# Performance work log

Hardware: AMD Instinct MI355X
Metric: run time of the kernel (lower is better)

The kernel has to match this reference:

```python
import jax, jax.numpy as jnp
import numpy as np

B, F, N, S, D = 128, 3, 64, 96, 64  # batch, features, nodes, steps, d_model
DIN = F + 1  # delta_t channel appended inside forward


def _layer_norm(x, g, b, eps=1e-5):
    mu = jnp.mean(x, -1, keepdims=True)
    var = jnp.mean((x - mu) ** 2, -1, keepdims=True)
    return (x - mu) * jax.lax.rsqrt(var + eps) * g + b


def _encoder_layer(x, inw, inb, ow, ob, w1, b1, w2, b2, g1, be1, g2, be2):
    # x: (B, N, D). Torch post-norm TransformerEncoderLayer, nhead=1, eval mode (no dropout).
    q, k, v = jnp.split(x @ inw.T + inb, 3, axis=-1)
    scores = jnp.einsum('bnd,bmd->bnm', q, k) / jnp.sqrt(jnp.asarray(D, x.dtype))
    a = jnp.einsum('bnm,bmd->bnd', jax.nn.softmax(scores, -1), v) @ ow.T + ob
    x = _layer_norm(x + a, g1, be1)
    ff = jax.nn.relu(x @ w1.T + b1) @ w2.T + b2
    return _layer_norm(x + ff, g2, be2)


def _diff_conv(x, adj, w, b):
    x1 = jnp.einsum('bcv,wv->bcw', x, adj)
    x2 = jnp.einsum('bcv,wv->bcw', x1, adj)
    z = jnp.concatenate([x, x1, x2], axis=1)  # (B, 3C, N)
    return jnp.einsum('bcn,oc->bon', z, w) + b[None, :, None]


def _forward(x, adj, h0, tp, uw, ub, cw, cb):
    times = x[:, 2, 0, :]  # (B, S) timestamps
    dt = jnp.concatenate([jnp.zeros((B, 1), x.dtype), times[:, 1:] - times[:, :-1]], axis=1)  # (B, S)
    xs = (jnp.transpose(x, (3, 0, 1, 2)), jnp.transpose(dt)[:, :, None])  # (S,B,F,N), (S,B,1)

    def step(h, inp):
        xt, d = inp  # (B,F,N), (B,1)
        xin = jnp.concatenate([xt, jnp.broadcast_to(d[:, :, None], (B, 1, N))], axis=1)  # (B,DIN,N)
        y = jnp.transpose(h, (0, 2, 1))  # (B, N, D): nodes are the attention sequence
        for i in range(2):
            y = _encoder_layer(y, *(a[i] for a in tp))
        eps = jnp.transpose(y, (0, 2, 1))  # (B, D, N)
        hd = jnp.sqrt(1.0 - d)[:, :, None] * h - jnp.sqrt(d)[:, :, None] * eps
        xg = jnp.concatenate([xin, hd], axis=1)  # (B, DIN+D, N)
        u = jax.nn.sigmoid(_diff_conv(xg, adj, uw, ub))
        c = jnp.tanh(_diff_conv(xg, adj, cw, cb))
        hn = u * hd + (1.0 - u) * c
        return hn, hn

    _, outs = jax.lax.scan(step, h0, xs)  # (S, B, D, N)
    return jnp.transpose(outs, (1, 3, 2, 0))  # (B, N, D, S) == stack().permute(1,3,2,0)


def setup_inputs() -> dict:
    key = jax.random.key(0)
    ks = jax.random.split(key, 12)
    s = 0.05
    x = jax.random.normal(ks[0], (B, F, N, S), jnp.float32)
    inc = jax.random.uniform(ks[1], (B, S), jnp.float32, 0.001, 0.01)
    x = x.at[:, 2, 0, :].set(jnp.cumsum(inc, axis=1))  # monotone times, delta_t in (0, 0.01)
    adj = jax.random.uniform(ks[2], (N, N), jnp.float32)
    adj = adj / jnp.sum(adj, axis=1, keepdims=True)
    h0 = jax.random.normal(ks[3], (B, D, N), jnp.float32)
    lengths = jax.random.randint(ks[4], (B,), 1, S, jnp.int32)  # unused by forward
    return {
        'x': x, 'adj': adj, 'lengths': lengths, 'h0': h0,
        't_inw': jax.random.normal(ks[5], (2, 3 * D, D), jnp.float32) * s,
        't_inb': jnp.zeros((2, 3 * D), jnp.float32),
        't_ow': jax.random.normal(ks[6], (2, D, D), jnp.float32) * s,
        't_ob': jnp.zeros((2, D), jnp.float32),
        't_w1': jax.random.normal(ks[7], (2, 64, D), jnp.float32) * s,
        't_b1': jnp.zeros((2, 64), jnp.float32),
        't_w2': jax.random.normal(ks[8], (2, D, 64), jnp.float32) * s,
        't_b2': jnp.zeros((2, D), jnp.float32),
        't_g1': jnp.ones((2, D), jnp.float32), 't_be1': jnp.zeros((2, D), jnp.float32),
        't_g2': jnp.ones((2, D), jnp.float32), 't_be2': jnp.zeros((2, D), jnp.float32),
        'uw': jax.random.normal(ks[9], (D, 3 * (DIN + D)), jnp.float32) * s,
        'ub': jnp.zeros((D,), jnp.float32),
        'cw': jax.random.normal(ks[10], (D, 3 * (DIN + D)), jnp.float32) * s,
        'cb': jnp.zeros((D,), jnp.float32),
    }


def reference(x, adj, lengths, h0, t_inw, t_inb, t_ow, t_ob, t_w1, t_b1, t_w2, t_b2,
              t_g1, t_be1, t_g2, t_be2, uw, ub, cw, cb):
    tp = (t_inw, t_inb, t_ow, t_ob, t_w1, t_b1, t_w2, t_b2, t_g1, t_be1, t_g2, t_be2)
    return _forward(x, adj, h0, tp, uw, ub, cw, cb)
```

## Files before the change

### kernel.cpp

```cpp
#include <hip/hip_runtime.h>
#include <math.h>

#define TPB 512

typedef __attribute__((ext_vector_type(8))) short bf16x8;
typedef __attribute__((ext_vector_type(4))) float f32x4;
typedef unsigned short u16;

#define MFMA(a, b, c) __builtin_amdgcn_mfma_f32_16x16x32_bf16(a, b, c, 0, 0, 0)

__device__ __forceinline__ u16 f2bf(float f) {
  union { float f; unsigned u; } v; v.f = f;
  unsigned u = v.u;
  return (u16)((u + 0x7fffu + ((u >> 16) & 1u)) >> 16);
}
__device__ __forceinline__ float bf2f(u16 h) {
  union { unsigned u; float f; } v; v.u = ((unsigned)h) << 16; return v.f;
}
__device__ __forceinline__ unsigned cvt2(float a0, float a1) {
  return (unsigned)f2bf(a0) | ((unsigned)f2bf(a1) << 16);
}
__device__ __forceinline__ void cvt4u(float a0, float a1, float a2, float a3, u16 o[4]) {
  o[0] = f2bf(a0); o[1] = f2bf(a1); o[2] = f2bf(a2); o[3] = f2bf(a3);
}

__device__ __forceinline__ bf16x8 fragL(const u16* B, int row0, int pitch, int kb, int lane) {
  return *(const bf16x8*)(B + (row0 + (lane & 15)) * pitch + kb + ((lane >> 4) << 3));
}
__device__ __forceinline__ bf16x8 fragG(const float* __restrict__ W, int row0, int stride,
                                        int kb, int lane) {
  const float* p = W + (size_t)(row0 + (lane & 15)) * stride + kb + ((lane >> 4) << 3);
  float4 a = *(const float4*)p, b = *(const float4*)(p + 4);
  bf16x8 r;
  r[0] = (short)f2bf(a.x); r[1] = (short)f2bf(a.y); r[2] = (short)f2bf(a.z); r[3] = (short)f2bf(a.w);
  r[4] = (short)f2bf(b.x); r[5] = (short)f2bf(b.y); r[6] = (short)f2bf(b.z); r[7] = (short)f2bf(b.w);
  return r;
}
template<int PREW>
__device__ __forceinline__ bf16x8 wfrag(const float* __restrict__ Wg,
                                        const u16* __restrict__ Wp,
                                        int m, int f, int kh, int lane) {
  if constexpr (PREW)
    return *(const bf16x8*)(Wp + (size_t)m * 4096 + f * 1024 + kh * 512 + lane * 8);
  else
    return fragG(Wg, f * 16, 64, kh * 32, lane);
}

__global__ __launch_bounds__(256)
void prep_kernel(const float* __restrict__ t_inw, const float* __restrict__ t_ow,
                 const float* __restrict__ t_w1, const float* __restrict__ t_w2,
                 const float* __restrict__ adj, const float* __restrict__ x,
                 u16* __restrict__ wp, u16* __restrict__ wpA2,
                 float* __restrict__ wsDT, u16* __restrict__ wsX) {
  int m = blockIdx.x;
  if (m == 12) {
    __shared__ float a2[4096];
    for (int e = threadIdx.x; e < 4096; e += 256) {
      int w = e >> 6, u = e & 63;
      float sum = 0.f;
      for (int v = 0; v < 64; ++v) sum += adj[w * 64 + v] * adj[v * 64 + u];
      a2[e] = sum;
    }
    __syncthreads();
    for (int t = threadIdx.x; t < 4096; t += 256) {
      int j = t & 7, ln = (t >> 3) & 63, kh = (t >> 9) & 1, f = t >> 10;
      int row = f * 16 + (ln & 15);
      int k = kh * 32 + ((ln >> 4) << 3) + j;
      wpA2[t] = f2bf(a2[row * 64 + k]);
    }
    return;
  }
  if (m >= 13) {
    int b = m - 13;
    const float* times = x + ((size_t)b * 3 + 2) * 64 * 96;
    for (int i = threadIdx.x; i < 96 * 256; i += 256) {
      int s = i >> 8, idx = i & 255, f = idx >> 6, n = idx & 63;
      float v;
      if (f < 3) v = x[(((size_t)b * 3 + f) * 64 + n) * 96 + s];
      else {
        float dt = s ? (times[s] - times[s - 1]) : 0.f;
        v = dt;
        if (n == 0) wsDT[b * 96 + s] = dt;
      }
      wsX[((size_t)b * 96 + s) * 256 + idx] = f2bf(v);
    }
    return;
  }
  int l = m / 6, r = m % 6;
  const float* W;
  if (r < 3)       W = t_inw + l * 12288 + r * 4096;
  else if (r == 3) W = t_ow + l * 4096;
  else if (r == 4) W = t_w1 + l * 4096;
  else             W = t_w2 + l * 4096;
  for (int t = threadIdx.x; t < 4096; t += 256) {
    int j = t & 7, ln = (t >> 3) & 63, kh = (t >> 9) & 1, f = t >> 10;
    int row = f * 16 + (ln & 15);
    int k = kh * 32 + ((ln >> 4) << 3) + j;
    wp[(size_t)m * 4096 + t] = f2bf(W[row * 64 + k]);
  }
}

__global__ __launch_bounds__(TPB, 2)
void gcrnn_fast(const float* __restrict__ adj,
                const float* __restrict__ h0,
                const float* __restrict__ t_inb, const float* __restrict__ t_ob,
                const float* __restrict__ t_b1,  const float* __restrict__ t_b2,
                const float* __restrict__ t_g1,  const float* __restrict__ t_be1,
                const float* __restrict__ t_g2,  const float* __restrict__ t_be2,
                const float* __restrict__ uw,    const float* __restrict__ ub,
                const float* __restrict__ cw,    const float* __restrict__ cb,
                const u16* __restrict__ wsW,  const u16* __restrict__ wsA2,
                const float* __restrict__ wsDT, const u16* __restrict__ wsX,
                float* __restrict__ wsOut)
{
  const int b = blockIdx.x;
  const int tid = threadIdx.x;
  const int wv = tid >> 6;
  const int lane = tid & 63;
  const int lx = lane & 15;
  const int gq = (lane >> 4) << 2;
  const int rs = wv & 3;
  const int of0 = (wv >> 2) * 2;
  const int fA = wv >> 2;

  __shared__ __align__(16) u16 adjB[64 * 72];
  __shared__ __align__(16) u16 Y0[64 * 72];
  __shared__ __align__(16) u16 Y1[64 * 72];
  __shared__ __align__(16) u16 Qb[64 * 72];
  __shared__ __align__(16) u16 Kb[64 * 72];
  __shared__ __align__(16) u16 VTb[64 * 72];
  __shared__ __align__(16) u16 Pb[64 * 72];
  __shared__ __align__(16) u16 xgB[80 * 72];
  __shared__ __align__(16) u16 zTB[64 * 232];
  __shared__ __align__(16) u16 uwcwB[2 * 4 * 7 * 512];

  float hreg[2][4];
  {
    const int nb = rs * 16 + gq;
#pragma unroll
    for (int ff = 0; ff < 2; ++ff) {
      int o = (of0 + ff) * 16 + lx;
      float4 hv = *(const float4*)(h0 + (size_t)b * 4096 + o * 64 + nb);
#pragma unroll
      for (int j = 0; j < 4; ++j) {
        hreg[ff][j] = (&hv.x)[j];
        Y0[(nb + j) * 72 + o] = f2bf(hreg[ff][j]);
      }
    }
  }
  for (int i = tid; i < 4096; i += TPB)
    adjB[(i >> 6) * 72 + (i & 63)] = f2bf(adj[i]);
  for (int i = tid; i < 2 * 4 * 7 * 512; i += TPB) {
    int t = i;
    int j = t & 7; t >>= 3;
    int ln = t & 63; t >>= 6;
    int kh = t % 7; t /= 7;
    int f = t & 3; int mat = t >> 2;
    int o = f * 16 + (ln & 15);
    int k = kh * 32 + ((ln >> 4) << 3) + j;
    const float* W = mat ? cw : uw;
    uwcwB[i] = (k < 204) ? f2bf(W[o * 204 + k]) : (u16)0;
  }
  for (int i = tid; i < 64 * 28; i += TPB)
    zTB[(i / 28) * 232 + 204 + (i % 28)] = 0;
  for (int i = tid; i < 12 * 72; i += TPB)
    xgB[68 * 72 + i] = 0;
  __syncthreads();

  const float buo = ub[of0 * 16 + lx], buo2 = ub[(of0 + 1) * 16 + lx];
  const float bco = cb[of0 * 16 + lx], bco2 = cb[(of0 + 1) * 16 + lx];
  float hdreg[2][4];

  for (int s = 0; s < 96; ++s) {
    float dcur = wsDT[b * 96 + s];
    float sq1 = sqrtf(1.f - dcur), sq2 = sqrtf(dcur);

    for (int l = 0; l < 2; ++l) {
      const int l6 = l * 6;
      const float* inb = t_inb + l * 192;
      const float* ob  = t_ob  + l * 64;
      const float* bb1 = t_b1  + l * 64;
      const float* bb2 = t_b2  + l * 64;
      const float* g1  = t_g1  + l * 64;
      const float* be1 = t_be1 + l * 64;
      const float* g2  = t_g2  + l * 64;
      const float* be2 = t_be2 + l * 64;

      bf16x8 fq[2][2], fk[2][2], fvr[2];
#pragma unroll
      for (int fi = 0; fi < 2; ++fi)
#pragma unroll
        for (int kh = 0; kh < 2; ++kh) {
          fq[fi][kh] = wfrag<1>(nullptr, wsW, l6 + 0, fA + fi * 2, kh, lane);
          fk[fi][kh] = wfrag<1>(nullptr, wsW, l6 + 1, fA + fi * 2, kh, lane);
        }
      if (wv >= 4) {
#pragma unroll
        for (int kh = 0; kh < 2; ++kh)
          fvr[kh] = wfrag<1>(nullptr, wsW, l6 + 2, rs, kh, lane);
      }

      {
        bf16x8 a0 = fragL(Y0, rs * 16, 72, 0, lane);
        bf16x8 a1 = fragL(Y0, rs * 16, 72, 32, lane);
#pragma unroll
        for (int fi = 0; fi < 2; ++fi) {
          int f = fA + fi * 2;
          int col = f * 16 + lx;
          {
            f32x4 acc = {0.f, 0.f, 0.f, 0.f};
            acc = MFMA(a0, fq[fi][0], acc);
            acc = MFMA(a1, fq[fi][1], acc);
            float bv = inb[col];
            u16 o4[4]; cvt4u(acc[0] + bv, acc[1] + bv, acc[2] + bv, acc[3] + bv, o4);
#pragma unroll
            for (int j = 0; j < 4; ++j)
              Qb[(rs * 16 + gq + j) * 72 + col] = o4[j];
          }
          {
            f32x4 acc = {0.f, 0.f, 0.f, 0.f};
            acc = MFMA(a0, fk[fi][0], acc);
            acc = MFMA(a1, fk[fi][1], acc);
            float bv = inb[64 + col];
            u16 o4[4]; cvt4u(acc[0] + bv, acc[1] + bv, acc[2] + bv, acc[3] + bv, o4);
#pragma unroll
            for (int j = 0; j < 4; ++j)
              Kb[(rs * 16 + gq + j) * 72 + col] = o4[j];
          }
        }
      }
      __syncthreads();

      if (wv < 4) {
        bf16x8 qa0 = fragL(Qb, rs * 16, 72, 0, lane);
        bf16x8 qa1 = fragL(Qb, rs * 16, 72, 32, lane);
        f32x4 sc[4];
#pragma unroll
        for (int f = 0; f < 4; ++f) {
          f32x4 acc = {0.f, 0.f, 0.f, 0.f};
          acc = MFMA(qa0, fragL(Kb, f * 16, 72, 0, lane), acc);
          acc = MFMA(qa1, fragL(Kb, f * 16, 72, 32, lane), acc);
#pragma unroll
          for (int j = 0; j < 4; ++j) acc[j] *= 0.125f;
          sc[f] = acc;
        }
#pragma unroll
        for (int j = 0; j < 4; ++j) {
          float m1 = fmaxf(fmaxf(sc[0][j], sc[1][j]), fmaxf(sc[2][j], sc[3][j]));
          m1 = fmaxf(m1, __shfl_xor(m1, 1));
          m1 = fmaxf(m1, __shfl_xor(m1, 2));
          m1 = fmaxf(m1, __shfl_xor(m1, 4));
          m1 = fmaxf(m1, __shfl_xor(m1, 8));
          float s1 = 0.f;
#pragma unroll
          for (int f = 0; f < 4; ++f) { float e = __expf(sc[f][j] - m1); sc[f][j] = e; s1 += e; }
          s1 += __shfl_xor(s1, 1); s1 += __shfl_xor(s1, 2);
          s1 += __shfl_xor(s1, 4); s1 += __shfl_xor(s1, 8);
          float inv = 1.f / s1;
          int row = rs * 16 + gq + j;
          u16 o4[4];
          cvt4u(sc[0][j] * inv, sc[1][j] * inv, sc[2][j] * inv, sc[3][j] * inv, o4);
#pragma unroll
          for (int f = 0; f < 4; ++f)
            Pb[row * 72 + f * 16 + lx] = o4[f];
        }
      } else {
#pragma unroll
        for (int f = 0; f < 4; ++f) {
          f32x4 acc = {0.f, 0.f, 0.f, 0.f};
          acc = MFMA(fvr[0], fragL(Y0, f * 16, 72, 0, lane), acc);
          acc = MFMA(fvr[1], fragL(Y0, f * 16, 72, 32, lane), acc);
          int dd0 = rs * 16 + gq;
          u16 o4[4];
          cvt4u(acc[0] + inb[128 + dd0], acc[1] + inb[128 + dd0 + 1],
                acc[2] + inb[128 + dd0 + 2], acc[3] + inb[128 + dd0 + 3], o4);
#pragma unroll
          for (int j = 0; j < 4; ++j)
            VTb[(dd0 + j) * 72 + f * 16 + lx] = o4[j];
        }
      }
      __syncthreads();

      if (wv < 4) {
        bf16x8 fo[4][2], fw1[4][2];
#pragma unroll
        for (int f = 0; f < 4; ++f)
#pragma unroll
          for (int kh = 0; kh < 2; ++kh) {
            fo[f][kh]  = wfrag<1>(nullptr, wsW, l6 + 3, f, kh, lane);
            fw1[f][kh] = wfrag<1>(nullptr, wsW, l6 + 4, f, kh, lane);
          }
        {
          bf16x8 pa0 = fragL(Pb, rs * 16, 72, 0, lane);
          bf16x8 pa1 = fragL(Pb, rs * 16, 72, 32, lane);
#pragma unroll
          for (int f = 0; f < 4; ++f) {
            f32x4 acc = {0.f, 0.f, 0.f, 0.f};
            acc = MFMA(pa0, fragL(VTb, f * 16, 72, 0, lane), acc);
            acc = MFMA(pa1, fragL(VTb, f * 16, 72, 32, lane), acc);
            u16 o4[4]; cvt4u(acc[0], acc[1], acc[2], acc[3], o4);
#pragma unroll
            for (int j = 0; j < 4; ++j)
              Qb[(rs * 16 + gq + j) * 72 + f * 16 + lx] = o4[j];
          }
        }
        {
          bf16x8 a0 = fragL(Qb, rs * 16, 72, 0, lane);
          bf16x8 a1 = fragL(Qb, rs * 16, 72, 32, lane);
          float t4[4][4];
#pragma unroll
          for (int f = 0; f < 4; ++f) {
            f32x4 acc = {0.f, 0.f, 0.f, 0.f};
            acc = MFMA(a0, fo[f][0], acc);
            acc = MFMA(a1, fo[f][1], acc);
            int col = f * 16 + lx;
            float bv = ob[col];
#pragma unroll
            for (int j = 0; j < 4; ++j) {
              int row = rs * 16 + gq + j;
              t4[f][j] = acc[j] + bv + bf2f(Y0[row * 72 + col]);
            }
          }
#pragma unroll
          for (int j = 0; j < 4; ++j) {
            float s1 = t4[0][j] + t4[1][j] + t4[2][j] + t4[3][j];
            float s2 = t4[0][j] * t4[0][j] + t4[1][j] * t4[1][j]
                     + t4[2][j] * t4[2][j] + t4[3][j] * t4[3][j];
            s1 += __shfl_xor(s1, 1); s2 += __shfl_xor(s2, 1);
            s1 += __shfl_xor(s1, 2); s2 += __shfl_xor(s2, 2);
            s1 += __shfl_xor(s1, 4); s2 += __shfl_xor(s2, 4);
            s1 += __shfl_xor(s1, 8); s2 += __shfl_xor(s2, 8);
            float mu = s1 * 0.015625f;
            float rstd = rsqrtf(s2 * 0.015625f - mu * mu + 1e-5f);
            int row = rs * 16 + gq + j;
            u16 o4[4];
            cvt4u((t4[0][j] - mu) * rstd * g1[0 * 16 + lx] + be1[0 * 16 + lx],
                  (t4[1][j] - mu) * rstd * g1[1 * 16 + lx] + be1[1 * 16 + lx],
                  (t4[2][j] - mu) * rstd * g1[2 * 16 + lx] + be1[2 * 16 + lx],
                  (t4[3][j] - mu) * rstd * g1[3 * 16 + lx] + be1[3 * 16 + lx], o4);
#pragma unroll
            for (int f = 0; f < 4; ++f)
              Y1[row * 72 + f * 16 + lx] = o4[f];
          }
        }
        {
          bf16x8 a0 = fragL(Y1, rs * 16, 72, 0, lane);
          bf16x8 a1 = fragL(Y1, rs * 16, 72, 32, lane);
#pragma unroll
          for (int f = 0; f < 4; ++f) {
            f32x4 acc = {0.f, 0.f, 0.f, 0.f};
            acc = MFMA(a0, fw1[f][0], acc);
            acc = MFMA(a1, fw1[f][1], acc);
            int col = f * 16 + lx;
            float bv = bb1[col];
            u16 o4[4];
            cvt4u(fmaxf(acc[0] + bv, 0.f), fmaxf(acc[1] + bv, 0.f),
                  fmaxf(acc[2] + bv, 0.f), fmaxf(acc[3] + bv, 0.f), o4);
#pragma unroll
            for (int j = 0; j < 4; ++j)
              Kb[(rs * 16 + gq + j) * 72 + col] = o4[j];
          }
        }
        if (l == 0) {
          bf16x8 fw2[4][2];
#pragma unroll
          for (int f = 0; f < 4; ++f)
#pragma unroll
            for (int kh = 0; kh < 2; ++kh)
              fw2[f][kh] = wfrag<1>(nullptr, wsW, l6 + 5, f, kh, lane);
          bf16x8 a0 = fragL(Kb, rs * 16, 72, 0, lane);
          bf16x8 a1 = fragL(Kb, rs * 16, 72, 32, lane);
          float t4[4][4];
#pragma unroll
          for (int f = 0; f < 4; ++f) {
            f32x4 acc = {0.f, 0.f, 0.f, 0.f};
            acc = MFMA(a0, fw2[f][0], acc);
            acc = MFMA(a1, fw2[f][1], acc);
            int col = f * 16 + lx;
            float bv = bb2[col];
#pragma unroll
            for (int j = 0; j < 4; ++j) {
              int row = rs * 16 + gq + j;
              t4[f][j] = acc[j] + bv + bf2f(Y1[row * 72 + col]);
            }
          }
#pragma unroll
          for (int j = 0; j < 4; ++j) {
            float s1 = t4[0][j] + t4[1][j] + t4[2][j] + t4[3][j];
            float s2 = t4[0][j] * t4[0][j] + t4[1][j] * t4[1][j]
                     + t4[2][j] * t4[2][j] + t4[3][j] * t4[3][j];
            s1 += __shfl_xor(s1, 1); s2 += __shfl_xor(s2, 1);
            s1 += __shfl_xor(s1, 2); s2 += __shfl_xor(s2, 2);
            s1 += __shfl_xor(s1, 4); s2 += __shfl_xor(s2, 4);
            s1 += __shfl_xor(s1, 8); s2 += __shfl_xor(s2, 8);
            float mu = s1 * 0.015625f;
            float rstd = rsqrtf(s2 * 0.015625f - mu * mu + 1e-5f);
            int row = rs * 16 + gq + j;
            u16 o4[4];
            cvt4u((t4[0][j] - mu) * rstd * g2[0 * 16 + lx] + be2[0 * 16 + lx],
                  (t4[1][j] - mu) * rstd * g2[1 * 16 + lx] + be2[1 * 16 + lx],
                  (t4[2][j] - mu) * rstd * g2[2 * 16 + lx] + be2[2 * 16 + lx],
                  (t4[3][j] - mu) * rstd * g2[3 * 16 + lx] + be2[3 * 16 + lx], o4);
#pragma unroll
            for (int f = 0; f < 4; ++f)
              Y0[row * 72 + f * 16 + lx] = o4[f];
          }
        }
      }
      __syncthreads();

      if (l == 1) {
        bf16x8 fw2[4][2];
#pragma unroll
        for (int f = 0; f < 4; ++f)
#pragma unroll
          for (int kh = 0; kh < 2; ++kh)
            fw2[f][kh] = wfrag<1>(nullptr, wsW, l6 + 5, f, kh, lane);
        bf16x8 a0 = fragL(Kb, rs * 16, 72, 0, lane);
        bf16x8 a1 = fragL(Kb, rs * 16, 72, 32, lane);
        float t4[4][4];
#pragma unroll
        for (int f = 0; f < 4; ++f) {
          f32x4 acc = {0.f, 0.f, 0.f, 0.f};
          acc = MFMA(a0, fw2[f][0], acc);
          acc = MFMA(a1, fw2[f][1], acc);
          int col = f * 16 + lx;
          float bv = bb2[col];
#pragma unroll
          for (int j = 0; j < 4; ++j) {
            int row = rs * 16 + gq + j;
            t4[f][j] = acc[j] + bv + bf2f(Y1[row * 72 + col]);
          }
        }
#pragma unroll
        for (int j = 0; j < 4; ++j) {
          float s1 = t4[0][j] + t4[1][j] + t4[2][j] + t4[3][j];
          float s2 = t4[0][j] * t4[0][j] + t4[1][j] * t4[1][j]
                   + t4[2][j] * t4[2][j] + t4[3][j] * t4[3][j];
          s1 += __shfl_xor(s1, 1); s2 += __shfl_xor(s2, 1);
          s1 += __shfl_xor(s1, 2); s2 += __shfl_xor(s2, 2);
          s1 += __shfl_xor(s1, 4); s2 += __shfl_xor(s2, 4);
          s1 += __shfl_xor(s1, 8); s2 += __shfl_xor(s2, 8);
          float mu = s1 * 0.015625f;
          float rstd = rsqrtf(s2 * 0.015625f - mu * mu + 1e-5f);
#pragma unroll
          for (int f = 0; f < 4; ++f) {
            int col = f * 16 + lx;
            t4[f][j] = (t4[f][j] - mu) * rstd * g2[col] + be2[col];
          }
        }
        {
          const u16* xr = wsX + ((size_t)b * 96 + s) * 256;
          for (int i = tid; i < 256; i += TPB) {
            u16 v = xr[i];
            int f = i >> 6, n = i & 63;
            xgB[f * 72 + n] = v;
            zTB[n * 232 + f] = v;
          }
        }
        const int nb = rs * 16 + gq;
#pragma unroll
        for (int f = 0; f < 4; ++f) {
          if ((f >> 1) == (wv >> 2)) {
            const int ff = f & 1;
            int o = f * 16 + lx;
            float hd0 = sq1 * hreg[ff][0] - sq2 * t4[f][0];
            float hd1 = sq1 * hreg[ff][1] - sq2 * t4[f][1];
            float hd2 = sq1 * hreg[ff][2] - sq2 * t4[f][2];
            float hd3 = sq1 * hreg[ff][3] - sq2 * t4[f][3];
            hdreg[ff][0] = hd0; hdreg[ff][1] = hd1;
            hdreg[ff][2] = hd2; hdreg[ff][3] = hd3;
            unsigned p0 = cvt2(hd0, hd1), p1 = cvt2(hd2, hd3);
            zTB[(nb + 0) * 232 + 4 + o] = (u16)p0;
            zTB[(nb + 1) * 232 + 4 + o] = (u16)(p0 >> 16);
            zTB[(nb + 2) * 232 + 4 + o] = (u16)p1;
            zTB[(nb + 3) * 232 + 4 + o] = (u16)(p1 >> 16);
            uint2 pk; pk.x = p0; pk.y = p1;
            *(uint2*)(xgB + (4 + o) * 72 + nb) = pk;
          }
        }
        __syncthreads();
      }
    }

    {
      f32x4 aU0 = {0.f,0.f,0.f,0.f}, aU1 = {0.f,0.f,0.f,0.f};
      f32x4 aC0 = {0.f,0.f,0.f,0.f}, aC1 = {0.f,0.f,0.f,0.f};
      bf16x8 g0 = *(const bf16x8*)(wsA2 + rs * 1024 + lane * 8);
      bf16x8 g1 = *(const bf16x8*)(wsA2 + rs * 1024 + 512 + lane * 8);
      bf16x8 aj0 = fragL(adjB, rs * 16, 72, 0, lane);
      bf16x8 aj1 = fragL(adjB, rs * 16, 72, 32, lane);

#define HT(A0, A1, CF, OFF) { \
      f32x4 acc = {0.f,0.f,0.f,0.f}; \
      acc = MFMA(A0, fragL(xgB, (CF) * 16, 72, 0, lane), acc); \
      acc = MFMA(A1, fragL(xgB, (CF) * 16, 72, 32, lane), acc); \
      int c = (CF) * 16 + lx; \
      if (c < 68) { u16 o4[4]; cvt4u(acc[0], acc[1], acc[2], acc[3], o4); \
        _Pragma("unroll") for (int j = 0; j < 4; ++j) \
          zTB[(rs * 16 + gq + j) * 232 + (OFF) + c] = o4[j]; } }

      HT(aj0, aj1, 0, 68); HT(aj0, aj1, 1, 68); HT(aj0, aj1, 2, 68);
      HT(aj0, aj1, 3, 68); HT(aj0, aj1, 4, 68);
#pragma unroll
      for (int kh = 0; kh < 2; ++kh) {
        bf16x8 a = fragL(zTB, rs * 16, 232, kh * 32, lane);
        {
          const u16* pu = uwcwB + (size_t)((of0 + 0) * 7 + kh) * 512 + lane * 8;
          const u16* pc = uwcwB + (size_t)((4 + of0 + 0) * 7 + kh) * 512 + lane * 8;
          aU0 = MFMA(a, *(const bf16x8*)pu, aU0);
          aC0 = MFMA(a, *(const bf16x8*)pc, aC0);
        }
        {
          const u16* pu = uwcwB + (size_t)((of0 + 1) * 7 + kh) * 512 + lane * 8;
          const u16* pc = uwcwB + (size_t)((4 + of0 + 1) * 7 + kh) * 512 + lane * 8;
          aU1 = MFMA(a, *(const bf16x8*)pu, aU1);
          aC1 = MFMA(a, *(const bf16x8*)pc, aC1);
        }
      }
      HT(g0, g1, 0, 136); HT(g0, g1, 1, 136); HT(g0, g1, 2, 136);
      HT(g0, g1, 3, 136); HT(g0, g1, 4, 136);
#undef HT

#pragma unroll
      for (int kh = 2; kh < 7; ++kh) {
        bf16x8 a = fragL(zTB, rs * 16, 232, kh * 32, lane);
        {
          const u16* pu = uwcwB + (size_t)((of0 + 0) * 7 + kh) * 512 + lane * 8;
          const u16* pc = uwcwB + (size_t)((4 + of0 + 0) * 7 + kh) * 512 + lane * 8;
          aU0 = MFMA(a, *(const bf16x8*)pu, aU0);
          aC0 = MFMA(a, *(const bf16x8*)pc, aC0);
        }
        {
          const u16* pu = uwcwB + (size_t)((of0 + 1) * 7 + kh) * 512 + lane * 8;
          const u16* pc = uwcwB + (size_t)((4 + of0 + 1) * 7 + kh) * 512 + lane * 8;
          aU1 = MFMA(a, *(const bf16x8*)pu, aU1);
          aC1 = MFMA(a, *(const bf16x8*)pc, aC1);
        }
      }
      const int nb = rs * 16 + gq;
#pragma unroll
      for (int ff = 0; ff < 2; ++ff) {
        f32x4 aU = ff ? aU1 : aU0;
        f32x4 aC = ff ? aC1 : aC0;
        float bu_ = ff ? buo2 : buo;
        float bc_ = ff ? bco2 : bco;
        int o = (of0 + ff) * 16 + lx;
        float4 ov;
#pragma unroll
        for (int j = 0; j < 4; ++j) {
          float u = 1.f / (1.f + __expf(-(aU[j] + bu_)));
          float z = aC[j] + bc_;
          z = fminf(fmaxf(z, -15.f), 15.f);
          float e2 = __expf(2.f * z);
          float cval = (e2 - 1.f) / (e2 + 1.f);
          float hn = u * hdreg[ff][j] + (1.f - u) * cval;
          hreg[ff][j] = hn;
          (&ov.x)[j] = hn;
        }
        unsigned pk0 = cvt2(ov.x, ov.y), pk1 = cvt2(ov.z, ov.w);
        Y0[(nb + 0) * 72 + o] = (u16)pk0;
        Y0[(nb + 1) * 72 + o] = (u16)(pk0 >> 16);
        Y0[(nb + 2) * 72 + o] = (u16)pk1;
        Y0[(nb + 3) * 72 + o] = (u16)(pk1 >> 16);
        *(float4*)(wsOut + ((size_t)b * 96 + s) * 4096 + o * 64 + nb) = ov;
      }
    }
    __syncthreads();
  }
}

__global__ __launch_bounds__(TPB, 2)
void gcrnn_fb(const float* __restrict__ x, const float* __restrict__ adj,
              const float* __restrict__ h0,
              const float* __restrict__ t_inw, const float* __restrict__ t_inb,
              const float* __restrict__ t_ow,  const float* __restrict__ t_ob,
              const float* __restrict__ t_w1,  const float* __restrict__ t_b1,
              const float* __restrict__ t_w2,  const float* __restrict__ t_b2,
              const float* __restrict__ t_g1,  const float* __restrict__ t_be1,
              const float* __restrict__ t_g2,  const float* __restrict__ t_be2,
              const float* __restrict__ uw,    const float* __restrict__ ub,
              const float* __restrict__ cw,    const float* __restrict__ cb,
              float* __restrict__ out)
{
  const int b = blockIdx.x;
  const int tid = threadIdx.x;
  const int wv = tid >> 6;
  const int lane = tid & 63;
  const int lx = lane & 15;
  const int gq = (lane >> 4) << 2;
  const int rs = wv & 3;
  const int of0 = (wv >> 2) * 2;
  const int fA = wv >> 2;

  __shared__ __align__(16) u16 adjB[64 * 72];
  __shared__ __align__(16) u16 adj2B[64 * 72];
  __shared__ __align__(16) u16 ysB[64 * 72];
  __shared__ __align__(16) u16 pool[4 * 4608];
  __shared__ __align__(16) u16 zTB[64 * 232];
  __shared__ __align__(16) u16 uwcwB[2 * 4 * 7 * 512];

  u16* Qb  = pool;
  u16* Kb  = pool + 4608;
  u16* VTb = pool + 9216;
  u16* Pb  = pool + 13824;
  u16* xgB = pool;

  float hreg[2][4];
  {
    const int nb = rs * 16 + gq;
#pragma unroll
    for (int ff = 0; ff < 2; ++ff) {
      int o = (of0 + ff) * 16 + lx;
      float4 hv = *(const float4*)(h0 + (size_t)b * 4096 + o * 64 + nb);
#pragma unroll
      for (int j = 0; j < 4; ++j) {
        hreg[ff][j] = (&hv.x)[j];
        ysB[(nb + j) * 72 + o] = f2bf(hreg[ff][j]);
      }
    }
  }
  for (int i = tid; i < 4096; i += TPB)
    adjB[(i >> 6) * 72 + (i & 63)] = f2bf(adj[i]);
  for (int i = tid; i < 4096; i += TPB) {
    int w = i >> 6, u = i & 63;
    float sum = 0.f;
    for (int v = 0; v < 64; ++v) sum += adj[w * 64 + v] * adj[v * 64 + u];
    adj2B[w * 72 + u] = f2bf(sum);
  }
  for (int i = tid; i < 2 * 4 * 7 * 512; i += TPB) {
    int t = i;
    int j = t & 7; t >>= 3;
    int ln = t & 63; t >>= 6;
    int kh = t % 7; t /= 7;
    int f = t & 3; int mat = t >> 2;
    int o = f * 16 + (ln & 15);
    int k = kh * 32 + ((ln >> 4) << 3) + j;
    const float* W = mat ? cw : uw;
    uwcwB[i] = (k < 204) ? f2bf(W[o * 204 + k]) : (u16)0;
  }
  for (int i = tid; i < 64 * 28; i += TPB)
    zTB[(i / 28) * 232 + 204 + (i % 28)] = 0;
  __syncthreads();

  const float* times = x + ((size_t)b * 3 + 2) * 64 * 96;
  float hdreg[2][4];

  for (int s = 0; s < 96; ++s) {
    float dcur = (s == 0) ? 0.f : (times[s] - times[s - 1]);
    float sq1 = sqrtf(1.f - dcur), sq2 = sqrtf(dcur);

    for (int l = 0; l < 2; ++l) {
      const float* inw = t_inw + l * 12288;
      const float* inb = t_inb + l * 192;
      const float* ow  = t_ow  + l * 4096;
      const float* ob  = t_ob  + l * 64;
      const float* w1  = t_w1  + l * 4096;
      const float* bb1 = t_b1  + l * 64;
      const float* w2  = t_w2  + l * 4096;
      const float* bb2 = t_b2  + l * 64;
      const float* g1  = t_g1  + l * 64;
      const float* be1 = t_be1 + l * 64;
      const float* g2  = t_g2  + l * 64;
      const float* be2 = t_be2 + l * 64;

      {
        bf16x8 a0 = fragL(ysB, rs * 16, 72, 0, lane);
        bf16x8 a1 = fragL(ysB, rs * 16, 72, 32, lane);
#pragma unroll
        for (int fi = 0; fi < 2; ++fi) {
          int f = fA + fi * 2;
          int col = f * 16 + lx;
          {
            f32x4 acc = {0.f, 0.f, 0.f, 0.f};
            acc = MFMA(a0, fragG(inw, f * 16, 64, 0, lane), acc);
            acc = MFMA(a1, fragG(inw, f * 16, 64, 32, lane), acc);
            float bv = inb[col];
            u16 o4[4]; cvt4u(acc[0] + bv, acc[1] + bv, acc[2] + bv, acc[3] + bv, o4);
#pragma unroll
            for (int j = 0; j < 4; ++j)
              Qb[(rs * 16 + gq + j) * 72 + col] = o4[j];
          }
          {
            f32x4 acc = {0.f, 0.f, 0.f, 0.f};
            acc = MFMA(a0, fragG(inw + 4096, f * 16, 64, 0, lane), acc);
            acc = MFMA(a1, fragG(inw + 4096, f * 16, 64, 32, lane), acc);
            float bv = inb[64 + col];
            u16 o4[4]; cvt4u(acc[0] + bv, acc[1] + bv, acc[2] + bv, acc[3] + bv, o4);
#pragma unroll
            for (int j = 0; j < 4; ++j)
              Kb[(rs * 16 + gq + j) * 72 + col] = o4[j];
          }
        }
      }
      __syncthreads();

      if (wv < 4) {
        bf16x8 qa0 = fragL(Qb, rs * 16, 72, 0, lane);
        bf16x8 qa1 = fragL(Qb, rs * 16, 72, 32, lane);
        f32x4 sc[4];
#pragma unroll
        for (int f = 0; f < 4; ++f) {
          f32x4 acc = {0.f, 0.f, 0.f, 0.f};
          acc = MFMA(qa0, fragL(Kb, f * 16, 72, 0, lane), acc);
          acc = MFMA(qa1, fragL(Kb, f * 16, 72, 32, lane), acc);
#pragma unroll
          for (int j = 0; j < 4; ++j) acc[j] *= 0.125f;
          sc[f] = acc;
        }
#pragma unroll
        for (int j = 0; j < 4; ++j) {
          float m1 = fmaxf(fmaxf(sc[0][j], sc[1][j]), fmaxf(sc[2][j], sc[3][j]));
          m1 = fmaxf(m1, __shfl_xor(m1, 1));
          m1 = fmaxf(m1, __shfl_xor(m1, 2));
          m1 = fmaxf(m1, __shfl_xor(m1, 4));
          m1 = fmaxf(m1, __shfl_xor(m1, 8));
          float s1 = 0.f;
#pragma unroll
          for (int f = 0; f < 4; ++f) { float e = __expf(sc[f][j] - m1); sc[f][j] = e; s1 += e; }
          s1 += __shfl_xor(s1, 1); s1 += __shfl_xor(s1, 2);
          s1 += __shfl_xor(s1, 4); s1 += __shfl_xor(s1, 8);
          float inv = 1.f / s1;
          int row = rs * 16 + gq + j;
          u16 o4[4];
          cvt4u(sc[0][j] * inv, sc[1][j] * inv, sc[2][j] * inv, sc[3][j] * inv, o4);
#pragma unroll
          for (int f = 0; f < 4; ++f)
            Pb[row * 72 + f * 16 + lx] = o4[f];
        }
      } else {
        bf16x8 wa0 = fragG(inw + 8192, rs * 16, 64, 0, lane);
        bf16x8 wa1 = fragG(inw + 8192, rs * 16, 64, 32, lane);
#pragma unroll
        for (int f = 0; f < 4; ++f) {
          f32x4 acc = {0.f, 0.f, 0.f, 0.f};
          acc = MFMA(wa0, fragL(ysB, f * 16, 72, 0, lane), acc);
          acc = MFMA(wa1, fragL(ysB, f * 16, 72, 32, lane), acc);
          int dd0 = rs * 16 + gq;
          u16 o4[4];
          cvt4u(acc[0] + inb[128 + dd0], acc[1] + inb[128 + dd0 + 1],
                acc[2] + inb[128 + dd0 + 2], acc[3] + inb[128 + dd0 + 3], o4);
#pragma unroll
          for (int j = 0; j < 4; ++j)
            VTb[(dd0 + j) * 72 + f * 16 + lx] = o4[j];
        }
      }
      __syncthreads();

      {
        bf16x8 pa0 = fragL(Pb, rs * 16, 72, 0, lane);
        bf16x8 pa1 = fragL(Pb, rs * 16, 72, 32, lane);
#pragma unroll
        for (int fi = 0; fi < 2; ++fi) {
          int f = fA + fi * 2;
          f32x4 acc = {0.f, 0.f, 0.f, 0.f};
          acc = MFMA(pa0, fragL(VTb, f * 16, 72, 0, lane), acc);
          acc = MFMA(pa1, fragL(VTb, f * 16, 72, 32, lane), acc);
          u16 o4[4]; cvt4u(acc[0], acc[1], acc[2], acc[3], o4);
#pragma unroll
          for (int j = 0; j < 4; ++j)
            Qb[(rs * 16 + gq + j) * 72 + f * 16 + lx] = o4[j];
        }
      }
      __syncthreads();

      if (wv < 4) {
        bf16x8 a0 = fragL(Qb, rs * 16, 72, 0, lane);
        bf16x8 a1 = fragL(Qb, rs * 16, 72, 32, lane);
        float t4[4][4];
#pragma unroll
        for (int f = 0; f < 4; ++f) {
          f32x4 acc = {0.f, 0.f, 0.f, 0.f};
          acc = MFMA(a0, fragG(ow, f * 16, 64, 0, lane), acc);
          acc = MFMA(a1, fragG(ow, f * 16, 64, 32, lane), acc);
          int col = f * 16 + lx;
          float bv = ob[col];
#pragma unroll
          for (int j = 0; j < 4; ++j) {
            int row = rs * 16 + gq + j;
            t4[f][j] = acc[j] + bv + bf2f(ysB[row * 72 + col]);
          }
        }
#pragma unroll
        for (int j = 0; j < 4; ++j) {
          float s1 = t4[0][j] + t4[1][j] + t4[2][j] + t4[3][j];
          float s2 = t4[0][j] * t4[0][j] + t4[1][j] * t4[1][j]
                   + t4[2][j] * t4[2][j] + t4[3][j] * t4[3][j];
          s1 += __shfl_xor(s1, 1); s2 += __shfl_xor(s2, 1);
          s1 += __shfl_xor(s1, 2); s2 += __shfl_xor(s2, 2);
          s1 += __shfl_xor(s1, 4); s2 += __shfl_xor(s2, 4);
          s1 += __shfl_xor(s1, 8); s2 += __shfl_xor(s2, 8);
          float mu = s1 * 0.015625f;
          float rstd = rsqrtf(s2 * 0.015625f - mu * mu + 1e-5f);
          int row = rs * 16 + gq + j;
          u16 o4[4];
          cvt4u((t4[0][j] - mu) * rstd * g1[0 * 16 + lx] + be1[0 * 16 + lx],
                (t4[1][j] - mu) * rstd * g1[1 * 16 + lx] + be1[1 * 16 + lx],
                (t4[2][j] - mu) * rstd * g1[2 * 16 + lx] + be1[2 * 16 + lx],
                (t4[3][j] - mu) * rstd * g1[3 * 16 + lx] + be1[3 * 16 + lx], o4);
#pragma unroll
          for (int f = 0; f < 4; ++f)
            ysB[row * 72 + f * 16 + lx] = o4[f];
        }
      }
      __syncthreads();

      {
        bf16x8 a0 = fragL(ysB, rs * 16, 72, 0, lane);
        bf16x8 a1 = fragL(ysB, rs * 16, 72, 32, lane);
#pragma unroll
        for (int fi = 0; fi < 2; ++fi) {
          int f = fA + fi * 2;
          f32x4 acc = {0.f, 0.f, 0.f, 0.f};
          acc = MFMA(a0, fragG(w1, f * 16, 64, 0, lane), acc);
          acc = MFMA(a1, fragG(w1, f * 16, 64, 32, lane), acc);
          int col = f * 16 + lx;
          float bv = bb1[col];
          u16 o4[4];
          cvt4u(fmaxf(acc[0] + bv, 0.f), fmaxf(acc[1] + bv, 0.f),
                fmaxf(acc[2] + bv, 0.f), fmaxf(acc[3] + bv, 0.f), o4);
#pragma unroll
          for (int j = 0; j < 4; ++j)
            Kb[(rs * 16 + gq + j) * 72 + col] = o4[j];
        }
      }
      __syncthreads();

      if (wv < 4) {
        bf16x8 a0 = fragL(Kb, rs * 16, 72, 0, lane);
        bf16x8 a1 = fragL(Kb, rs * 16, 72, 32, lane);
        float t4[4][4];
#pragma unroll
        for (int f = 0; f < 4; ++f) {
          f32x4 acc = {0.f, 0.f, 0.f, 0.f};
          acc = MFMA(a0, fragG(w2, f * 16, 64, 0, lane), acc);
          acc = MFMA(a1, fragG(w2, f * 16, 64, 32, lane), acc);
          int col = f * 16 + lx;
          float bv = bb2[col];
#pragma unroll
          for (int j = 0; j < 4; ++j) {
            int row = rs * 16 + gq + j;
            t4[f][j] = acc[j] + bv + bf2f(ysB[row * 72 + col]);
          }
        }
#pragma unroll
        for (int j = 0; j < 4; ++j) {
          float s1 = t4[0][j] + t4[1][j] + t4[2][j] + t4[3][j];
          float s2 = t4[0][j] * t4[0][j] + t4[1][j] * t4[1][j]
                   + t4[2][j] * t4[2][j] + t4[3][j] * t4[3][j];
          s1 += __shfl_xor(s1, 1); s2 += __shfl_xor(s2, 1);
          s1 += __shfl_xor(s1, 2); s2 += __shfl_xor(s2, 2);
          s1 += __shfl_xor(s1, 4); s2 += __shfl_xor(s2, 4);
          s1 += __shfl_xor(s1, 8); s2 += __shfl_xor(s2, 8);
          float mu = s1 * 0.015625f;
          float rstd = rsqrtf(s2 * 0.015625f - mu * mu + 1e-5f);
          int row = rs * 16 + gq + j;
          u16 o4[4];
          cvt4u((t4[0][j] - mu) * rstd * g2[0 * 16 + lx] + be2[0 * 16 + lx],
                (t4[1][j] - mu) * rstd * g2[1 * 16 + lx] + be2[1 * 16 + lx],
                (t4[2][j] - mu) * rstd * g2[2 * 16 + lx] + be2[2 * 16 + lx],
                (t4[3][j] - mu) * rstd * g2[3 * 16 + lx] + be2[3 * 16 + lx], o4);
#pragma unroll
          for (int f = 0; f < 4; ++f)
            ysB[row * 72 + f * 16 + lx] = o4[f];
        }
      }
      __syncthreads();
    }

    {
      for (int i = tid; i < 256; i += TPB) {
        int f = i >> 6, n = i & 63;
        float v = (f < 3) ? x[(((size_t)b * 3 + f) * 64 + n) * 96 + s] : dcur;
        u16 v16 = f2bf(v);
        xgB[f * 72 + n] = v16;
        zTB[n * 232 + f] = v16;
      }
      const int nb = rs * 16 + gq;
#pragma unroll
      for (int ff = 0; ff < 2; ++ff) {
        int o = (of0 + ff) * 16 + lx;
        float hd0 = sq1 * hreg[ff][0] - sq2 * bf2f(ysB[(nb + 0) * 72 + o]);
        float hd1 = sq1 * hreg[ff][1] - sq2 * bf2f(ysB[(nb + 1) * 72 + o]);
        float hd2 = sq1 * hreg[ff][2] - sq2 * bf2f(ysB[(nb + 2) * 72 + o]);
        float hd3 = sq1 * hreg[ff][3] - sq2 * bf2f(ysB[(nb + 3) * 72 + o]);
        hdreg[ff][0] = hd0; hdreg[ff][1] = hd1; hdreg[ff][2] = hd2; hdreg[ff][3] = hd3;
        unsigned p0 = cvt2(hd0, hd1), p1 = cvt2(hd2, hd3);
        zTB[(nb + 0) * 232 + 4 + o] = (u16)p0;
        zTB[(nb + 1) * 232 + 4 + o] = (u16)(p0 >> 16);
        zTB[(nb + 2) * 232 + 4 + o] = (u16)p1;
        zTB[(nb + 3) * 232 + 4 + o] = (u16)(p1 >> 16);
        uint2 pk; pk.x = p0; pk.y = p1;
        *(uint2*)(xgB + (4 + o) * 72 + nb) = pk;
      }
    }
    __syncthreads();

    for (int t = wv; t < 40; t += 8) {
      int which = (t >= 20) ? 1 : 0;
      int tt = t - which * 20;
      int rw = tt & 3, cf = tt >> 2;
      const u16* A = which ? adj2B : adjB;
      f32x4 acc = {0.f, 0.f, 0.f, 0.f};
      acc = MFMA(fragL(A, rw * 16, 72, 0, lane), fragL(xgB, cf * 16, 72, 0, lane), acc);
      acc = MFMA(fragL(A, rw * 16, 72, 32, lane), fragL(xgB, cf * 16, 72, 32, lane), acc);
      int c = cf * 16 + lx;
      if (c < 68) {
        u16 o4[4]; cvt4u(acc[0], acc[1], acc[2], acc[3], o4);
#pragma unroll
        for (int j = 0; j < 4; ++j)
          zTB[(rw * 16 + gq + j) * 232 + 68 + which * 68 + c] = o4[j];
      }
    }
    __syncthreads();

    {
      f32x4 aU[2] = {{0.f,0.f,0.f,0.f},{0.f,0.f,0.f,0.f}};
      f32x4 aC[2] = {{0.f,0.f,0.f,0.f},{0.f,0.f,0.f,0.f}};
#pragma unroll
      for (int kh = 0; kh < 7; ++kh) {
        bf16x8 a = fragL(zTB, rs * 16, 232, kh * 32, lane);
#pragma unroll
        for (int ff = 0; ff < 2; ++ff) {
          int f = of0 + ff;
          const u16* pu = uwcwB + (size_t)((0 * 4 + f) * 7 + kh) * 512 + lane * 8;
          const u16* pc = uwcwB + (size_t)((1 * 4 + f) * 7 + kh) * 512 + lane * 8;
          aU[ff] = MFMA(a, *(const bf16x8*)pu, aU[ff]);
          aC[ff] = MFMA(a, *(const bf16x8*)pc, aC[ff]);
        }
      }
      const int nb = rs * 16 + gq;
#pragma unroll
      for (int ff = 0; ff < 2; ++ff) {
        int o = (of0 + ff) * 16 + lx;
        float bu_ = ub[o], bc_ = cb[o];
        float4 ov;
#pragma unroll
        for (int j = 0; j < 4; ++j) {
          float u = 1.f / (1.f + __expf(-(aU[ff][j] + bu_)));
          float z = aC[ff][j] + bc_;
          z = fminf(fmaxf(z, -15.f), 15.f);
          float e2 = __expf(2.f * z);
          float cval = (e2 - 1.f) / (e2 + 1.f);
          float hn = u * hdreg[ff][j] + (1.f - u) * cval;
          hreg[ff][j] = hn;
          (&ov.x)[j] = hn;
        }
        unsigned pk0 = cvt2(ov.x, ov.y), pk1 = cvt2(ov.z, ov.w);
        ysB[(nb + 0) * 72 + o] = (u16)pk0;
        ysB[(nb + 1) * 72 + o] = (u16)(pk0 >> 16);
        ysB[(nb + 2) * 72 + o] = (u16)pk1;
        ysB[(nb + 3) * 72 + o] = (u16)(pk1 >> 16);
#pragma unroll
        for (int j = 0; j < 4; ++j)
          out[((size_t)(b * 64 + (nb + j)) * 64 + o) * 96 + s] = (&ov.x)[j];
      }
    }
    __syncthreads();
  }
}

__global__ __launch_bounds__(256)
void transp_kernel(const float* __restrict__ ws, float* __restrict__ out) {
  int blk = blockIdx.x;
  int b = blk >> 6, o = blk & 63;
  __shared__ float t[96 * 68];
  for (int i = threadIdx.x; i < 96 * 64; i += 256) {
    int ss = i >> 6, n = i & 63;
    t[ss * 68 + n] = ws[((size_t)b * 96 + ss) * 4096 + o * 64 + n];
  }
  __syncthreads();
  for (int i = threadIdx.x; i < 64 * 96; i += 256) {
    int n = i / 96, ss = i - n * 96;
    out[((size_t)(b * 64 + n) * 64 + o) * 96 + ss] = t[ss * 68 + n];
  }
}

extern "C" void kernel_launch(void* const* d_in, const int* in_sizes, int n_in,
                              void* d_out, int out_size, void* d_ws, size_t ws_size,
                              hipStream_t stream)
{
  (void)in_sizes; (void)n_in; (void)out_size;
  const float* x     = (const float*)d_in[0];
  const float* adj   = (const float*)d_in[1];
  const float* h0    = (const float*)d_in[3];
  const float* t_inw = (const float*)d_in[4];
  const float* t_inb = (const float*)d_in[5];
  const float* t_ow  = (const float*)d_in[6];
  const float* t_ob  = (const float*)d_in[7];
  const float* t_w1  = (const float*)d_in[8];
  const float* t_b1  = (const float*)d_in[9];
  const float* t_w2  = (const float*)d_in[10];
  const float* t_b2  = (const float*)d_in[11];
  const float* t_g1  = (const float*)d_in[12];
  const float* t_be1 = (const float*)d_in[13];
  const float* t_g2  = (const float*)d_in[14];
  const float* t_be2 = (const float*)d_in[15];
  const float* uw    = (const float*)d_in[16];
  const float* ub    = (const float*)d_in[17];
  const float* cw    = (const float*)d_in[18];
  const float* cb    = (const float*)d_in[19];
  float* out = (float*)d_out;

  const size_t offA2    = 98304;
  const size_t offDT    = 106496;
  const size_t offX     = 155648;
  const size_t offStage = 6447104;
  const size_t stageBytes = (size_t)128 * 96 * 4096 * 4;

  if (ws_size >= offStage + stageBytes) {
    u16*   wsW   = (u16*)d_ws;
    u16*   wsA2  = (u16*)((char*)d_ws + offA2);
    float* wsDT  = (float*)((char*)d_ws + offDT);
    u16*   wsX   = (u16*)((char*)d_ws + offX);
    float* wsOut = (float*)((char*)d_ws + offStage);

    hipLaunchKernelGGL(prep_kernel, dim3(141), dim3(256), 0, stream,
                       t_inw, t_ow, t_w1, t_w2, adj, x, wsW, wsA2, wsDT, wsX);
    hipLaunchKernelGGL(gcrnn_fast, dim3(128), dim3(TPB), 0, stream,
                       adj, h0, t_inb, t_ob, t_b1, t_b2, t_g1, t_be1, t_g2, t_be2,
                       uw, ub, cw, cb, wsW, wsA2, wsDT, wsX, wsOut);
    hipLaunchKernelGGL(transp_kernel, dim3(128 * 64), dim3(256), 0, stream, wsOut, out);
  } else {
    hipLaunchKernelGGL(gcrnn_fb, dim3(128), dim3(TPB), 0, stream,
                       x, adj, h0, t_inw, t_inb, t_ow, t_ob, t_w1, t_b1,
                       t_w2, t_b2, t_g1, t_be1, t_g2, t_be2, uw, ub, cw, cb, out);
  }
}
```

Before: 1.447 ms.

## Rebalance QKV projection across waves and drop a per-layer barrier

Waves 0-3 now compute all of Q plus half of K, while waves 4-7 compute the other half of K and V^T in the same phase. V^T is therefore ready at the first barrier, so the separate barrier after the score/softmax phase is removed. The attention-output and FFN weight fragment loads are hoisted earlier to overlap latency. The FFN hidden buffer moves from Kb to Pb to avoid a hazard now that Kb is still being read. The bf16 conversion is also swapped for the HIP library intrinsic. Extra registers for the hoisted fragments may raise register pressure.

```diff
diff --git a/kernel.cpp b/kernel.cpp
--- a/kernel.cpp
+++ b/kernel.cpp
@@ -1,4 +1,5 @@
 #include <hip/hip_runtime.h>
+#include <hip/hip_bf16.h>
 #include <math.h>
 
 #define TPB 512
@@ -10,9 +11,8 @@
 #define MFMA(a, b, c) __builtin_amdgcn_mfma_f32_16x16x32_bf16(a, b, c, 0, 0, 0)
 
 __device__ __forceinline__ u16 f2bf(float f) {
-  union { float f; unsigned u; } v; v.f = f;
-  unsigned u = v.u;
-  return (u16)((u + 0x7fffu + ((u >> 16) & 1u)) >> 16);
+  __hip_bfloat16 h = __float2bfloat16(f);
+  return *reinterpret_cast<u16*>(&h);
 }
 __device__ __forceinline__ float bf2f(u16 h) {
   union { unsigned u; float f; } v; v.u = ((unsigned)h) << 16; return v.f;
@@ -121,7 +121,6 @@
   const int gq = (lane >> 4) << 2;
   const int rs = wv & 3;
   const int of0 = (wv >> 2) * 2;
-  const int fA = wv >> 2;
 
   __shared__ __align__(16) u16 adjB[64 * 72];
   __shared__ __align__(16) u16 Y0[64 * 72];
@@ -186,64 +185,107 @@
       const float* g2  = t_g2  + l * 64;
       const float* be2 = t_be2 + l * 64;
 
-      bf16x8 fq[2][2], fk[2][2], fvr[2];
-#pragma unroll
-      for (int fi = 0; fi < 2; ++fi)
-#pragma unroll
-        for (int kh = 0; kh < 2; ++kh) {
-          fq[fi][kh] = wfrag<1>(nullptr, wsW, l6 + 0, fA + fi * 2, kh, lane);
-          fk[fi][kh] = wfrag<1>(nullptr, wsW, l6 + 1, fA + fi * 2, kh, lane);
-        }
-      if (wv >= 4) {
-#pragma unroll
-        for (int kh = 0; kh < 2; ++kh)
-          fvr[kh] = wfrag<1>(nullptr, wsW, l6 + 2, rs, kh, lane);
-      }
-
       {
         bf16x8 a0 = fragL(Y0, rs * 16, 72, 0, lane);
         bf16x8 a1 = fragL(Y0, rs * 16, 72, 32, lane);
-#pragma unroll
-        for (int fi = 0; fi < 2; ++fi) {
-          int f = fA + fi * 2;
-          int col = f * 16 + lx;
-          {
+        if (wv < 4) {
+          bf16x8 fq[4][2], fkp[2][2];
+#pragma unroll
+          for (int f = 0; f < 4; ++f)
+#pragma unroll
+            for (int kh = 0; kh < 2; ++kh)
+              fq[f][kh] = wfrag<1>(nullptr, wsW, l6 + 0, f, kh, lane);
+#pragma unroll
+          for (int fi = 0; fi < 2; ++fi)
+#pragma unroll
+            for (int kh = 0; kh < 2; ++kh)
+              fkp[fi][kh] = wfrag<1>(nullptr, wsW, l6 + 1, fi * 2, kh, lane);
+#pragma unroll
+          for (int f = 0; f < 4; ++f) {
             f32x4 acc = {0.f, 0.f, 0.f, 0.f};
-            acc = MFMA(a0, fq[fi][0], acc);
-            acc = MFMA(a1, fq[fi][1], acc);
+            acc = MFMA(a0, fq[f][0], acc);
+            acc = MFMA(a1, fq[f][1], acc);
+            int col = f * 16 + lx;
             float bv = inb[col];
             u16 o4[4]; cvt4u(acc[0] + bv, acc[1] + bv, acc[2] + bv, acc[3] + bv, o4);
 #pragma unroll
             for (int j = 0; j < 4; ++j)
               Qb[(rs * 16 + gq + j) * 72 + col] = o4[j];
           }
-          {
+#pragma unroll
+          for (int fi = 0; fi < 2; ++fi) {
+            int f = fi * 2;
             f32x4 acc = {0.f, 0.f, 0.f, 0.f};
-            acc = MFMA(a0, fk[fi][0], acc);
-            acc = MFMA(a1, fk[fi][1], acc);
+            acc = MFMA(a0, fkp[fi][0], acc);
+            acc = MFMA(a1, fkp[fi][1], acc);
+            int col = f * 16 + lx;
             float bv = inb[64 + col];
             u16 o4[4]; cvt4u(acc[0] + bv, acc[1] + bv, acc[2] + bv, acc[3] + bv, o4);
 #pragma unroll
             for (int j = 0; j < 4; ++j)
               Kb[(rs * 16 + gq + j) * 72 + col] = o4[j];
           }
+        } else {
+          bf16x8 fkp[2][2], fvr[2];
+#pragma unroll
+          for (int fi = 0; fi < 2; ++fi)
+#pragma unroll
+            for (int kh = 0; kh < 2; ++kh)
+              fkp[fi][kh] = wfrag<1>(nullptr, wsW, l6 + 1, 1 + fi * 2, kh, lane);
+#pragma unroll
+          for (int kh = 0; kh < 2; ++kh)
+            fvr[kh] = wfrag<1>(nullptr, wsW, l6 + 2, rs, kh, lane);
+#pragma unroll
+          for (int fi = 0; fi < 2; ++fi) {
+            int f = 1 + fi * 2;
+            f32x4 acc = {0.f, 0.f, 0.f, 0.f};
+            acc = MFMA(a0, fkp[fi][0], acc);
+            acc = MFMA(a1, fkp[fi][1], acc);
+            int col = f * 16 + lx;
+            float bv = inb[64 + col];
+            u16 o4[4]; cvt4u(acc[0] + bv, acc[1] + bv, acc[2] + bv, acc[3] + bv, o4);
+#pragma unroll
+            for (int j = 0; j < 4; ++j)
+              Kb[(rs * 16 + gq + j) * 72 + col] = o4[j];
+          }
+#pragma unroll
+          for (int f = 0; f < 4; ++f) {
+            f32x4 acc = {0.f, 0.f, 0.f, 0.f};
+            acc = MFMA(fvr[0], fragL(Y0, f * 16, 72, 0, lane), acc);
+            acc = MFMA(fvr[1], fragL(Y0, f * 16, 72, 32, lane), acc);
+            int dd0 = rs * 16 + gq;
+            u16 o4[4];
+            cvt4u(acc[0] + inb[128 + dd0], acc[1] + inb[128 + dd0 + 1],
+                  acc[2] + inb[128 + dd0 + 2], acc[3] + inb[128 + dd0 + 3], o4);
+#pragma unroll
+            for (int j = 0; j < 4; ++j)
+              VTb[(dd0 + j) * 72 + f * 16 + lx] = o4[j];
+          }
         }
       }
       __syncthreads();
 
       if (wv < 4) {
-        bf16x8 qa0 = fragL(Qb, rs * 16, 72, 0, lane);
-        bf16x8 qa1 = fragL(Qb, rs * 16, 72, 32, lane);
         f32x4 sc[4];
-#pragma unroll
-        for (int f = 0; f < 4; ++f) {
-          f32x4 acc = {0.f, 0.f, 0.f, 0.f};
-          acc = MFMA(qa0, fragL(Kb, f * 16, 72, 0, lane), acc);
-          acc = MFMA(qa1, fragL(Kb, f * 16, 72, 32, lane), acc);
-#pragma unroll
-          for (int j = 0; j < 4; ++j) acc[j] *= 0.125f;
-          sc[f] = acc;
-        }
+        {
+          bf16x8 qa0 = fragL(Qb, rs * 16, 72, 0, lane);
+          bf16x8 qa1 = fragL(Qb, rs * 16, 72, 32, lane);
+#pragma unroll
+          for (int f = 0; f < 4; ++f) {
+            f32x4 acc = {0.f, 0.f, 0.f, 0.f};
+            acc = MFMA(qa0, fragL(Kb, f * 16, 72, 0, lane), acc);
+            acc = MFMA(qa1, fragL(Kb, f * 16, 72, 32, lane), acc);
+#pragma unroll
+            for (int j = 0; j < 4; ++j) acc[j] *= 0.125f;
+            sc[f] = acc;
+          }
+        }
+        bf16x8 fo[4][2];
+#pragma unroll
+        for (int f = 0; f < 4; ++f)
+#pragma unroll
+          for (int kh = 0; kh < 2; ++kh)
+            fo[f][kh] = wfrag<1>(nullptr, wsW, l6 + 3, f, kh, lane);
 #pragma unroll
         for (int j = 0; j < 4; ++j) {
           float m1 = fmaxf(fmaxf(sc[0][j], sc[1][j]), fmaxf(sc[2][j], sc[3][j]));
@@ -264,32 +306,12 @@
           for (int f = 0; f < 4; ++f)
             Pb[row * 72 + f * 16 + lx] = o4[f];
         }
-      } else {
-#pragma unroll
-        for (int f = 0; f < 4; ++f) {
-          f32x4 acc = {0.f, 0.f, 0.f, 0.f};
-          acc = MFMA(fvr[0], fragL(Y0, f * 16, 72, 0, lane), acc);
-          acc = MFMA(fvr[1], fragL(Y0, f * 16, 72, 32, lane), acc);
-          int dd0 = rs * 16 + gq;
-          u16 o4[4];
-          cvt4u(acc[0] + inb[128 + dd0], acc[1] + inb[128 + dd0 + 1],
-                acc[2] + inb[128 + dd0 + 2], acc[3] + inb[128 + dd0 + 3], o4);
-#pragma unroll
-          for (int j = 0; j < 4; ++j)
-            VTb[(dd0 + j) * 72 + f * 16 + lx] = o4[j];
-        }
-      }
-      __syncthreads();
-
-      if (wv < 4) {
-        bf16x8 fo[4][2], fw1[4][2];
+        bf16x8 fw1[4][2];
 #pragma unroll
         for (int f = 0; f < 4; ++f)
 #pragma unroll
-          for (int kh = 0; kh < 2; ++kh) {
-            fo[f][kh]  = wfrag<1>(nullptr, wsW, l6 + 3, f, kh, lane);
+          for (int kh = 0; kh < 2; ++kh)
             fw1[f][kh] = wfrag<1>(nullptr, wsW, l6 + 4, f, kh, lane);
-          }
         {
           bf16x8 pa0 = fragL(Pb, rs * 16, 72, 0, lane);
           bf16x8 pa1 = fragL(Pb, rs * 16, 72, 32, lane);
@@ -303,6 +325,14 @@
             for (int j = 0; j < 4; ++j)
               Qb[(rs * 16 + gq + j) * 72 + f * 16 + lx] = o4[j];
           }
+        }
+        bf16x8 fw2[4][2];
+        if (l == 0) {
+#pragma unroll
+          for (int f = 0; f < 4; ++f)
+#pragma unroll
+            for (int kh = 0; kh < 2; ++kh)
+              fw2[f][kh] = wfrag<1>(nullptr, wsW, l6 + 5, f, kh, lane);
         }
         {
           bf16x8 a0 = fragL(Qb, rs * 16, 72, 0, lane);
@@ -358,18 +388,12 @@
                   fmaxf(acc[2] + bv, 0.f), fmaxf(acc[3] + bv, 0.f), o4);
 #pragma unroll
             for (int j = 0; j < 4; ++j)
-              Kb[(rs * 16 + gq + j) * 72 + col] = o4[j];
+              Pb[(rs * 16 + gq + j) * 72 + col] = o4[j];
           }
         }
         if (l == 0) {
-          bf16x8 fw2[4][2];
-#pragma unroll
-          for (int f = 0; f < 4; ++f)
-#pragma unroll
-            for (int kh = 0; kh < 2; ++kh)
-              fw2[f][kh] = wfrag<1>(nullptr, wsW, l6 + 5, f, kh, lane);
-          bf16x8 a0 = fragL(Kb, rs * 16, 72, 0, lane);
-          bf16x8 a1 = fragL(Kb, rs * 16, 72, 32, lane);
+          bf16x8 a0 = fragL(Pb, rs * 16, 72, 0, lane);
+          bf16x8 a1 = fragL(Pb, rs * 16, 72, 32, lane);
           float t4[4][4];
 #pragma unroll
           for (int f = 0; f < 4; ++f) {
@@ -416,8 +440,8 @@
 #pragma unroll
           for (int kh = 0; kh < 2; ++kh)
             fw2[f][kh] = wfrag<1>(nullptr, wsW, l6 + 5, f, kh, lane);
-        bf16x8 a0 = fragL(Kb, rs * 16, 72, 0, lane);
-        bf16x8 a1 = fragL(Kb, rs * 16, 72, 32, lane);
+        bf16x8 a0 = fragL(Pb, rs * 16, 72, 0, lane);
+        bf16x8 a1 = fragL(Pb, rs * 16, 72, 32, lane);
         float t4[4][4];
 #pragma unroll
         for (int f = 0; f < 4; ++f) {
```

Measured after the change: 1.561 ms. +7.9%, slower.
